# Optimization experiments

Hardware: AMD Instinct MI355X
Metric: run time of the kernel (lower is better)

Reference implementation:

```python
import jax, jax.numpy as jnp
import numpy as np

B, D, CTX, H = 8192, 64, 256, 512  # batch, latent dim (made.nin), context dim, MADE hidden


def _masks(D, H):
    """Standard MADE natural-ordering masks (Germain et al. 2015)."""
    m0 = np.arange(1, D + 1)                 # input degrees 1..D
    mh = (np.arange(H) % (D - 1)) + 1        # hidden degrees 1..D-1
    M1 = (mh[:, None] >= m0[None, :]).astype(np.float32)   # (H, D)
    M2 = (mh[:, None] >= mh[None, :]).astype(np.float32)   # (H, H)
    mo = np.concatenate([m0, m0])            # outputs = [means; pre_scales]
    Mo = (mo[:, None] > mh[None, :]).astype(np.float32)    # (2D, H)
    return jnp.asarray(M1), jnp.asarray(M2), jnp.asarray(Mo)


def setup_inputs() -> dict:
    key = jax.random.key(0)
    ks = jax.random.split(key, 7)
    s = 0.05
    return {
        "context": jax.random.normal(ks[0], (B, CTX), jnp.float32),
        "eps": jax.random.normal(ks[1], (B, D), jnp.float32),  # reparameterization noise
        "W1": jax.random.normal(ks[2], (H, D), jnp.float32) * s,
        "b1": jnp.zeros((H,), jnp.float32),
        "Wc": jax.random.normal(ks[3], (H, CTX), jnp.float32) * s,
        "W2": jax.random.normal(ks[4], (H, H), jnp.float32) * s,
        "b2": jnp.zeros((H,), jnp.float32),
        "Wo": jax.random.normal(ks[5], (2 * D, H), jnp.float32) * s,
        "bo": jnp.zeros((2 * D,), jnp.float32),
    }


def reference(context, eps, W1, b1, Wc, W2, b2, Wo, bo):
    """AutoRegressiveDistribution.rsample (gaussian): D sequential MADE forwards,
    each extracting column i of (mu, softplus(pre_scale)) and sampling z_i."""
    M1, M2, Mo = _masks(D, H)
    W1m, W2m, Wom = (W1 * M1).T, (W2 * M2).T, (Wo * Mo).T
    ctx_h = context @ Wc.T  # context projection is constant across steps

    def step(z, i):
        h = jax.nn.relu(z @ W1m + ctx_h + b1)   # (B, H)
        h = jax.nn.relu(h @ W2m + b2)           # (B, H)
        out = h @ Wom + bo                      # (B, 2D): [means | pre_scales]
        mu_i = out[:, i]
        scale_i = jax.nn.softplus(out[:, D + i])
        z_i = mu_i + scale_i * eps[:, i]        # Normal(mu, scale).rsample()
        z = z.at[:, i].set(z_i)
        return z, (mu_i, scale_i)

    z0 = jnp.zeros((context.shape[0], D), context.dtype)
    z, (mus, scales) = jax.lax.scan(step, z0, jnp.arange(D))
    # state = (z_sample, mu_inferred, scale_inferred), each (B, D)
    return z, mus.T, scales.T
```

## Files before the change

### kernel.cpp

```cpp
#include <hip/hip_runtime.h>
#include <math.h>


typedef float f2 __attribute__((ext_vector_type(2)));

#define Bn 8192
#define Dn 64
#define CTXn 256
#define Hn 512
#define On 128
#define Rn 8

#define WQ_SZ  (64 * 512 * 12)
#define WOQ_SZ (64 * 64 * 20)
#define WCP_SZ (CTXn * Hn)

__device__ __forceinline__ int S_of(int k) {
  if (k <= 0) return 0;
  if (k <= 9) return 9 * (k - 1);
  return 72 + 8 * (k - 9);
}
__device__ __forceinline__ int perm_of(int p, int* degout) {
  int k, t;
  if (p < 72) { k = p / 9 + 1; t = p - (k - 1) * 9; }
  else        { int pp = p - 72; k = pp / 8 + 9; t = pp - (k - 9) * 8; }
  *degout = k;
  return (k - 1) + 63 * t;
}

__global__ void prep_kernel(const float* __restrict__ W1, const float* __restrict__ Wc,
                            const float* __restrict__ W2, const float* __restrict__ Wo,
                            const float* __restrict__ b1, const float* __restrict__ b2,
                            float* __restrict__ Wq, float* __restrict__ Woq,
                            float* __restrict__ WcpT, float* __restrict__ b1p,
                            float* __restrict__ b2p) {
  int idx = blockIdx.x * 256 + threadIdx.x;
  if (idx < WQ_SZ) {
    int i = idx / 6144, rem = idx - i * 6144;
    int q = rem / 12, e = rem - q * 12;
    int sb = (i < 8) ? 9 * i : 8 * i + 8;
    int c  = (i == 63) ? 0 : ((i < 8) ? 9 : 8);
    int dq; int hq = perm_of(q, &dq);
    float v = 0.f;
    if (e < 9) {
      if (e < c && dq >= i + 1) {
        int dp; int hp = perm_of(sb + e, &dp);
        v = W2[hq * Hn + hp];
      }
    } else if (e == 9) {
      if (dq >= i + 1) v = W1[hq * Dn + i];
    }
    Wq[idx] = v;
  } else if (idx < WQ_SZ + WOQ_SZ) {
    int jj = idx - WQ_SZ;
    int i = jj / 1280, rem = jj - i * 1280;
    int j = rem / 20, e = rem - j * 20;
    int sb = (i < 8) ? 9 * i : 8 * i + 8;
    int c  = (i == 63) ? 0 : ((i < 8) ? 9 : 8);
    float v = 0.f;
    int p = -1, o = 0;
    if (e < 9)                { p = e;      o = j; }
    else if (e >= 10 && e < 19) { p = e - 10; o = j + 64; }
    if (p >= 0 && p < c && j >= i + 1) {
      int dp; int hp = perm_of(sb + p, &dp);
      v = Wo[o * Hn + hp];
    }
    Woq[jj] = v;
  } else if (idx < WQ_SZ + WOQ_SZ + WCP_SZ) {
    int jj = idx - (WQ_SZ + WOQ_SZ);
    int cc = jj >> 9, q = jj & 511;
    int dq; int hq = perm_of(q, &dq);
    WcpT[jj] = Wc[hq * CTXn + cc];
  } else if (idx < WQ_SZ + WOQ_SZ + WCP_SZ + 512) {
    int q = idx - (WQ_SZ + WOQ_SZ + WCP_SZ);
    int dq; int hq = perm_of(q, &dq);
    b1p[q] = b1[hq];
  } else if (idx < WQ_SZ + WOQ_SZ + WCP_SZ + 1024) {
    int q = idx - (WQ_SZ + WOQ_SZ + WCP_SZ + 512);
    int dq; int hq = perm_of(q, &dq);
    b2p[q] = b2[hq];
  }
}

__global__ __launch_bounds__(256, 4)
void made_pk_kernel(
    const float* __restrict__ context, const float* __restrict__ WcpT,
    const float* __restrict__ b1p,
    const float* __restrict__ Wq, const float* __restrict__ Woq,
    const float* __restrict__ b2p, const float* __restrict__ bo,
    const float* __restrict__ eps, float* __restrict__ out) {
  __shared__ __align__(16) float ctxR[8][264];
  __shared__ __align__(16) float zcur[8];
  __shared__ __align__(16) float h1g[9][8];
  __shared__ __align__(16) float h2g[9][8];

  int t = threadIdx.x;
  int b0 = blockIdx.x * Rn;
  int rp = t >> 6, l = t & 63;
  int q0 = t, q1 = t + 256;

  int g0 = ((q0 < 72) ? q0 / 9 + 1 : (q0 - 72) / 8 + 9) - 1;
  int g1 = ((q1 - 72) / 8 + 9) - 1;
  int qm = t | 63;
  int gm0s = __builtin_amdgcn_readfirstlane(
      ((qm < 72) ? qm / 9 + 1 : (qm - 72) / 8 + 9) - 1);
  int gm1s = __builtin_amdgcn_readfirstlane(((qm + 256 - 72) / 8 + 9) - 1);

  #pragma unroll
  for (int r = 0; r < 8; ++r)
    ctxR[r][t] = context[(b0 + r) * CTXn + t];
  __syncthreads();

  float acc0[8], acc1[8];
  {
    float bias0 = b1p[q0], bias1 = b1p[q1];
    #pragma unroll
    for (int r = 0; r < 8; ++r) { acc0[r] = bias0; acc1[r] = bias1; }
  }
  {
    const float* wc = WcpT;
    #pragma clang loop unroll(disable)
    for (int c4 = 0; c4 < CTXn / 4; ++c4) {
      float xr[8][4];
      #pragma unroll
      for (int r = 0; r < 8; ++r) {
        float4 x = *(const float4*)&ctxR[r][4 * c4];
        xr[r][0] = x.x; xr[r][1] = x.y; xr[r][2] = x.z; xr[r][3] = x.w;
      }
      #pragma unroll
      for (int k = 0; k < 4; ++k) {
        float w0 = wc[q0], w1 = wc[q1];
        #pragma unroll
        for (int r = 0; r < 8; ++r) {
          acc0[r] = fmaf(xr[r][k], w0, acc0[r]);
          acc1[r] = fmaf(xr[r][k], w1, acc1[r]);
        }
        wc += Hn;
      }
    }
  }

  f2 a10[4], a11[4], a20[4], a21[4];
  #pragma unroll
  for (int r2 = 0; r2 < 4; ++r2) {
    a10[r2] = (f2){acc0[2 * r2], acc0[2 * r2 + 1]};
    a11[r2] = (f2){acc1[2 * r2], acc1[2 * r2 + 1]};
  }
  {
    float bb0 = b2p[q0], bb1 = b2p[q1];
    #pragma unroll
    for (int r2 = 0; r2 < 4; ++r2) {
      a20[r2] = (f2){bb0, bb0};
      a21[r2] = (f2){bb1, bb1};
    }
  }
  f2 ocA = (f2){bo[l], bo[l]};
  f2 ocB = (f2){bo[l + 64], bo[l + 64]};
  f2 ez2 = (f2){eps[(b0 + 2 * rp) * Dn + l], eps[(b0 + 2 * rp + 1) * Dn + l]};
  f2 zs = (f2){0.f, 0.f}, mus = zs, scs = zs;

  const float* wq0p = Wq + (size_t)q0 * 12;
  const float* wq1p = Wq + (size_t)q1 * 12;
  const float* wopp = Woq + (size_t)l * 20;

  #pragma clang loop unroll(disable)
  for (int i = 0; i < Dn; ++i) {
    if (l == i) {
      f2 pre = ocB;
      float sx = fmaxf(pre.x, 0.f) + __logf(1.f + __expf(-fabsf(pre.x)));
      float sy = fmaxf(pre.y, 0.f) + __logf(1.f + __expf(-fabsf(pre.y)));
      f2 sc = (f2){sx, sy};
      f2 z = ocA + sc * ez2;
      *(f2*)&zcur[2 * rp] = z;
      zs = z; mus = ocA; scs = sc;
    }
    __syncthreads();

    int sb = (i < 8) ? 9 * i : 8 * i + 8;
    bool liveB = (i <= gm1s);
    bool liveA = (i <= gm0s);
    float4 A1c0, A1c1, A1c2, A0c0, A0c1, A0c2;
    if (liveB) {
      const float4* a4 = (const float4*)wq1p;
      A1c0 = a4[0]; A1c1 = a4[1]; A1c2 = a4[2];
      if (liveA) {
        const float4* b4 = (const float4*)wq0p;
        A0c0 = b4[0]; A0c1 = b4[1]; A0c2 = b4[2];
      }
      float4 za = *(const float4*)&zcur[0];
      float4 zb = *(const float4*)&zcur[4];
      f2 zc0 = (f2){za.x, za.y}, zc1 = (f2){za.z, za.w};
      f2 zc2 = (f2){zb.x, zb.y}, zc3 = (f2){zb.z, zb.w};
      {
        f2 wv = (f2){A1c2.y, A1c2.y};
        a11[0] += wv * zc0; a11[1] += wv * zc1;
        a11[2] += wv * zc2; a11[3] += wv * zc3;
        if (g1 == i) {
          int pp = q1 - sb;
          float4 h0 = {fmaxf(a11[0].x, 0.f), fmaxf(a11[0].y, 0.f),
                       fmaxf(a11[1].x, 0.f), fmaxf(a11[1].y, 0.f)};
          float4 h1_ = {fmaxf(a11[2].x, 0.f), fmaxf(a11[2].y, 0.f),
                        fmaxf(a11[3].x, 0.f), fmaxf(a11[3].y, 0.f)};
          *(float4*)&h1g[pp][0] = h0; *(float4*)&h1g[pp][4] = h1_;
        }
      }
      if (liveA) {
        f2 wv = (f2){A0c2.y, A0c2.y};
        a10[0] += wv * zc0; a10[1] += wv * zc1;
        a10[2] += wv * zc2; a10[3] += wv * zc3;
        if (g0 == i) {
          int pp = q0 - sb;
          float4 h0 = {fmaxf(a10[0].x, 0.f), fmaxf(a10[0].y, 0.f),
                       fmaxf(a10[1].x, 0.f), fmaxf(a10[1].y, 0.f)};
          float4 h1_ = {fmaxf(a10[2].x, 0.f), fmaxf(a10[2].y, 0.f),
                        fmaxf(a10[3].x, 0.f), fmaxf(a10[3].y, 0.f)};
          *(float4*)&h1g[pp][0] = h0; *(float4*)&h1g[pp][4] = h1_;
        }
      }
    }
    __syncthreads();

    const float4* w4 = (const float4*)wopp;
    float4 B0 = w4[0], B1 = w4[1], B2 = w4[2], B3 = w4[3], B4 = w4[4];

    if (liveB) {
      float wA1[9] = {A1c0.x, A1c0.y, A1c0.z, A1c0.w,
                      A1c1.x, A1c1.y, A1c1.z, A1c1.w, A1c2.x};
      if (liveA) {
        float wA0[9] = {A0c0.x, A0c0.y, A0c0.z, A0c0.w,
                        A0c1.x, A0c1.y, A0c1.z, A0c1.w, A0c2.x};
        #pragma unroll
        for (int p = 0; p < 9; ++p) {
          float4 ha = *(const float4*)&h1g[p][0];
          float4 hb = *(const float4*)&h1g[p][4];
          f2 h0 = (f2){ha.x, ha.y}, h1_ = (f2){ha.z, ha.w};
          f2 h2_ = (f2){hb.x, hb.y}, h3 = (f2){hb.z, hb.w};
          f2 wv1 = (f2){wA1[p], wA1[p]};
          f2 wv0 = (f2){wA0[p], wA0[p]};
          a21[0] += wv1 * h0; a21[1] += wv1 * h1_;
          a21[2] += wv1 * h2_; a21[3] += wv1 * h3;
          a20[0] += wv0 * h0; a20[1] += wv0 * h1_;
          a20[2] += wv0 * h2_; a20[3] += wv0 * h3;
        }
      } else {
        #pragma unroll
        for (int p = 0; p < 9; ++p) {
          float4 ha = *(const float4*)&h1g[p][0];
          float4 hb = *(const float4*)&h1g[p][4];
          f2 h0 = (f2){ha.x, ha.y}, h1_ = (f2){ha.z, ha.w};
          f2 h2_ = (f2){hb.x, hb.y}, h3 = (f2){hb.z, hb.w};
          f2 wv1 = (f2){wA1[p], wA1[p]};
          a21[0] += wv1 * h0; a21[1] += wv1 * h1_;
          a21[2] += wv1 * h2_; a21[3] += wv1 * h3;
        }
      }
      if (g1 == i) {
        int pp = q1 - sb;
        float4 h0 = {fmaxf(a21[0].x, 0.f), fmaxf(a21[0].y, 0.f),
                     fmaxf(a21[1].x, 0.f), fmaxf(a21[1].y, 0.f)};
        float4 h1_ = {fmaxf(a21[2].x, 0.f), fmaxf(a21[2].y, 0.f),
                      fmaxf(a21[3].x, 0.f), fmaxf(a21[3].y, 0.f)};
        *(float4*)&h2g[pp][0] = h0; *(float4*)&h2g[pp][4] = h1_;
      }
      if (liveA && g0 == i) {
        int pp = q0 - sb;
        float4 h0 = {fmaxf(a20[0].x, 0.f), fmaxf(a20[0].y, 0.f),
                     fmaxf(a20[1].x, 0.f), fmaxf(a20[1].y, 0.f)};
        float4 h1_ = {fmaxf(a20[2].x, 0.f), fmaxf(a20[2].y, 0.f),
                      fmaxf(a20[3].x, 0.f), fmaxf(a20[3].y, 0.f)};
        *(float4*)&h2g[pp][0] = h0; *(float4*)&h2g[pp][4] = h1_;
      }
    }
    __syncthreads();

    {
      float wBa[9] = {B0.x, B0.y, B0.z, B0.w, B1.x, B1.y, B1.z, B1.w, B2.x};
      float wBb[9] = {B2.z, B2.w, B3.x, B3.y, B3.z, B3.w, B4.x, B4.y, B4.z};
      #pragma unroll
      for (int p = 0; p < 9; ++p) {
        f2 h = *(const f2*)&h2g[p][2 * rp];
        ocA += (f2){wBa[p], wBa[p]} * h;
        ocB += (f2){wBb[p], wBb[p]} * h;
      }
    }
    wq0p += 6144; wq1p += 6144; wopp += 1280;
  }

  out[(b0 + 2 * rp) * Dn + l] = zs.x;
  out[(b0 + 2 * rp + 1) * Dn + l] = zs.y;
  out[Bn * Dn + (b0 + 2 * rp) * Dn + l] = mus.x;
  out[Bn * Dn + (b0 + 2 * rp + 1) * Dn + l] = mus.y;
  out[2 * Bn * Dn + (b0 + 2 * rp) * Dn + l] = scs.x;
  out[2 * Bn * Dn + (b0 + 2 * rp + 1) * Dn + l] = scs.y;
}

extern "C" void kernel_launch(void* const* d_in, const int* in_sizes, int n_in,
                              void* d_out, int out_size, void* d_ws, size_t ws_size,
                              hipStream_t stream) {
  const float* context = (const float*)d_in[0];
  const float* eps     = (const float*)d_in[1];
  const float* W1      = (const float*)d_in[2];
  const float* b1      = (const float*)d_in[3];
  const float* Wc      = (const float*)d_in[4];
  const float* W2      = (const float*)d_in[5];
  const float* b2      = (const float*)d_in[6];
  const float* Wo      = (const float*)d_in[7];
  const float* bo      = (const float*)d_in[8];
  float* out = (float*)d_out;

  float* ws   = (float*)d_ws;
  float* Wq   = ws;
  float* Woq  = Wq + WQ_SZ;
  float* WcpT = Woq + WOQ_SZ;
  float* b1p  = WcpT + WCP_SZ;
  float* b2p  = b1p + 512;

  int prep_elems = WQ_SZ + WOQ_SZ + WCP_SZ + 1024;
  prep_kernel<<<(prep_elems + 255) / 256, 256, 0, stream>>>(
      W1, Wc, W2, Wo, b1, b2, Wq, Woq, WcpT, b1p, b2p);
  made_pk_kernel<<<Bn / Rn, 256, 0, stream>>>(context, WcpT, b1p, Wq, Woq,
                                              b2p, bo, eps, out);
}
```

Baseline: 239.2 us.

## Use 512-thread blocks with one hidden unit per thread over 16 rows

Reorganizes the per-block work so each of 512 threads owns a single hidden unit and accumulates over 16 batch rows, where before 256 threads each owned two units over 8 rows. Grid size halves and weight loads per row are amortized over twice as many rows. Each step's early-exit liveness check is now per wave on a single unit. The output stage still indexes 64 lanes by 2*rp rows, and with rp ranging 0..7 this covers the 16 rows. The cost is more accumulator registers per thread and larger barrier groups.

```diff
diff --git a/kernel.cpp b/kernel.cpp
--- a/kernel.cpp
+++ b/kernel.cpp
@@ -9,17 +9,12 @@
 #define CTXn 256
 #define Hn 512
 #define On 128
-#define Rn 8
+#define Rn 16
 
 #define WQ_SZ  (64 * 512 * 12)
 #define WOQ_SZ (64 * 64 * 20)
 #define WCP_SZ (CTXn * Hn)
 
-__device__ __forceinline__ int S_of(int k) {
-  if (k <= 0) return 0;
-  if (k <= 9) return 9 * (k - 1);
-  return 72 + 8 * (k - 9);
-}
 __device__ __forceinline__ int perm_of(int p, int* degout) {
   int k, t;
   if (p < 72) { k = p / 9 + 1; t = p - (k - 1) * 9; }
@@ -59,7 +54,7 @@
     int c  = (i == 63) ? 0 : ((i < 8) ? 9 : 8);
     float v = 0.f;
     int p = -1, o = 0;
-    if (e < 9)                { p = e;      o = j; }
+    if (e < 9)                  { p = e;      o = j; }
     else if (e >= 10 && e < 19) { p = e - 10; o = j + 64; }
     if (p >= 0 && p < c && j >= i + 1) {
       int dp; int hp = perm_of(sb + p, &dp);
@@ -82,85 +77,76 @@
   }
 }
 
-__global__ __launch_bounds__(256, 4)
+__global__ __launch_bounds__(512, 2)
 void made_pk_kernel(
     const float* __restrict__ context, const float* __restrict__ WcpT,
     const float* __restrict__ b1p,
     const float* __restrict__ Wq, const float* __restrict__ Woq,
     const float* __restrict__ b2p, const float* __restrict__ bo,
     const float* __restrict__ eps, float* __restrict__ out) {
-  __shared__ __align__(16) float ctxR[8][264];
-  __shared__ __align__(16) float zcur[8];
-  __shared__ __align__(16) float h1g[9][8];
-  __shared__ __align__(16) float h2g[9][8];
+  __shared__ __align__(16) float ctxR[Rn][264];
+  __shared__ __align__(16) float zcur[Rn];
+  __shared__ __align__(16) float h1g[9][Rn];
+  __shared__ __align__(16) float h2g[9][Rn];
 
   int t = threadIdx.x;
   int b0 = blockIdx.x * Rn;
-  int rp = t >> 6, l = t & 63;
-  int q0 = t, q1 = t + 256;
-
-  int g0 = ((q0 < 72) ? q0 / 9 + 1 : (q0 - 72) / 8 + 9) - 1;
-  int g1 = ((q1 - 72) / 8 + 9) - 1;
+  int q = t;
+  int l = t & 63, rp = t >> 6;
+
+  int fstep = (q < 72) ? q / 9 : (q - 72) / 8 + 8;
   int qm = t | 63;
-  int gm0s = __builtin_amdgcn_readfirstlane(
-      ((qm < 72) ? qm / 9 + 1 : (qm - 72) / 8 + 9) - 1);
-  int gm1s = __builtin_amdgcn_readfirstlane(((qm + 256 - 72) / 8 + 9) - 1);
-
-  #pragma unroll
-  for (int r = 0; r < 8; ++r)
-    ctxR[r][t] = context[(b0 + r) * CTXn + t];
+  int gmax = __builtin_amdgcn_readfirstlane(
+      (qm < 72) ? qm / 9 : (qm - 72) / 8 + 8);
+
+  for (int idx = t; idx < Rn * CTXn; idx += 512) {
+    int r = idx >> 8, cc = idx & 255;
+    ctxR[r][cc] = context[(b0 + r) * CTXn + cc];
+  }
   __syncthreads();
 
-  float acc0[8], acc1[8];
+  float acc[Rn];
   {
-    float bias0 = b1p[q0], bias1 = b1p[q1];
+    float bias = b1p[q];
     #pragma unroll
-    for (int r = 0; r < 8; ++r) { acc0[r] = bias0; acc1[r] = bias1; }
-  }
-  {
+    for (int r = 0; r < Rn; ++r) acc[r] = bias;
+  }
+  #pragma clang loop unroll(disable)
+  for (int half = 0; half < 2; ++half) {
     const float* wc = WcpT;
     #pragma clang loop unroll(disable)
     for (int c4 = 0; c4 < CTXn / 4; ++c4) {
       float xr[8][4];
       #pragma unroll
       for (int r = 0; r < 8; ++r) {
-        float4 x = *(const float4*)&ctxR[r][4 * c4];
+        float4 x = *(const float4*)&ctxR[8 * half + r][4 * c4];
         xr[r][0] = x.x; xr[r][1] = x.y; xr[r][2] = x.z; xr[r][3] = x.w;
       }
       #pragma unroll
       for (int k = 0; k < 4; ++k) {
-        float w0 = wc[q0], w1 = wc[q1];
-        #pragma unroll
-        for (int r = 0; r < 8; ++r) {
-          acc0[r] = fmaf(xr[r][k], w0, acc0[r]);
-          acc1[r] = fmaf(xr[r][k], w1, acc1[r]);
-        }
+        float w0 = wc[q];
+        #pragma unroll
+        for (int r = 0; r < 8; ++r)
+          acc[8 * half + r] = fmaf(xr[r][k], w0, acc[8 * half + r]);
         wc += Hn;
       }
     }
   }
 
-  f2 a10[4], a11[4], a20[4], a21[4];
+  f2 a1[8], a2[8];
   #pragma unroll
-  for (int r2 = 0; r2 < 4; ++r2) {
-    a10[r2] = (f2){acc0[2 * r2], acc0[2 * r2 + 1]};
-    a11[r2] = (f2){acc1[2 * r2], acc1[2 * r2 + 1]};
-  }
+  for (int r2 = 0; r2 < 8; ++r2) a1[r2] = (f2){acc[2 * r2], acc[2 * r2 + 1]};
   {
-    float bb0 = b2p[q0], bb1 = b2p[q1];
+    float bb = b2p[q];
     #pragma unroll
-    for (int r2 = 0; r2 < 4; ++r2) {
-      a20[r2] = (f2){bb0, bb0};
-      a21[r2] = (f2){bb1, bb1};
-    }
+    for (int r2 = 0; r2 < 8; ++r2) a2[r2] = (f2){bb, bb};
   }
   f2 ocA = (f2){bo[l], bo[l]};
   f2 ocB = (f2){bo[l + 64], bo[l + 64]};
   f2 ez2 = (f2){eps[(b0 + 2 * rp) * Dn + l], eps[(b0 + 2 * rp + 1) * Dn + l]};
   f2 zs = (f2){0.f, 0.f}, mus = zs, scs = zs;
 
-  const float* wq0p = Wq + (size_t)q0 * 12;
-  const float* wq1p = Wq + (size_t)q1 * 12;
+  const float* wqp = Wq + (size_t)q * 12;
   const float* wopp = Woq + (size_t)l * 20;
 
   #pragma clang loop unroll(disable)
@@ -177,44 +163,28 @@
     __syncthreads();
 
     int sb = (i < 8) ? 9 * i : 8 * i + 8;
-    bool liveB = (i <= gm1s);
-    bool liveA = (i <= gm0s);
-    float4 A1c0, A1c1, A1c2, A0c0, A0c1, A0c2;
-    if (liveB) {
-      const float4* a4 = (const float4*)wq1p;
-      A1c0 = a4[0]; A1c1 = a4[1]; A1c2 = a4[2];
-      if (liveA) {
-        const float4* b4 = (const float4*)wq0p;
-        A0c0 = b4[0]; A0c1 = b4[1]; A0c2 = b4[2];
-      }
+    bool live = (i <= gmax);
+    float4 A0, A1, A2;
+    if (live) {
+      const float4* a4 = (const float4*)wqp;
+      A0 = a4[0]; A1 = a4[1]; A2 = a4[2];
       float4 za = *(const float4*)&zcur[0];
       float4 zb = *(const float4*)&zcur[4];
-      f2 zc0 = (f2){za.x, za.y}, zc1 = (f2){za.z, za.w};
-      f2 zc2 = (f2){zb.x, zb.y}, zc3 = (f2){zb.z, zb.w};
-      {
-        f2 wv = (f2){A1c2.y, A1c2.y};
-        a11[0] += wv * zc0; a11[1] += wv * zc1;
-        a11[2] += wv * zc2; a11[3] += wv * zc3;
-        if (g1 == i) {
-          int pp = q1 - sb;
-          float4 h0 = {fmaxf(a11[0].x, 0.f), fmaxf(a11[0].y, 0.f),
-                       fmaxf(a11[1].x, 0.f), fmaxf(a11[1].y, 0.f)};
-          float4 h1_ = {fmaxf(a11[2].x, 0.f), fmaxf(a11[2].y, 0.f),
-                        fmaxf(a11[3].x, 0.f), fmaxf(a11[3].y, 0.f)};
-          *(float4*)&h1g[pp][0] = h0; *(float4*)&h1g[pp][4] = h1_;
-        }
-      }
-      if (liveA) {
-        f2 wv = (f2){A0c2.y, A0c2.y};
-        a10[0] += wv * zc0; a10[1] += wv * zc1;
-        a10[2] += wv * zc2; a10[3] += wv * zc3;
-        if (g0 == i) {
-          int pp = q0 - sb;
-          float4 h0 = {fmaxf(a10[0].x, 0.f), fmaxf(a10[0].y, 0.f),
-                       fmaxf(a10[1].x, 0.f), fmaxf(a10[1].y, 0.f)};
-          float4 h1_ = {fmaxf(a10[2].x, 0.f), fmaxf(a10[2].y, 0.f),
-                        fmaxf(a10[3].x, 0.f), fmaxf(a10[3].y, 0.f)};
-          *(float4*)&h1g[pp][0] = h0; *(float4*)&h1g[pp][4] = h1_;
+      float4 zc_ = *(const float4*)&zcur[8];
+      float4 zd = *(const float4*)&zcur[12];
+      f2 zc[8] = {(f2){za.x, za.y}, (f2){za.z, za.w},
+                  (f2){zb.x, zb.y}, (f2){zb.z, zb.w},
+                  (f2){zc_.x, zc_.y}, (f2){zc_.z, zc_.w},
+                  (f2){zd.x, zd.y}, (f2){zd.z, zd.w}};
+      f2 wv = (f2){A2.y, A2.y};
+      #pragma unroll
+      for (int r2 = 0; r2 < 8; ++r2) a1[r2] += wv * zc[r2];
+      if (fstep == i) {
+        int pp = q - sb;
+        #pragma unroll
+        for (int r2 = 0; r2 < 8; ++r2) {
+          f2 h = (f2){fmaxf(a1[r2].x, 0.f), fmaxf(a1[r2].y, 0.f)};
+          *(f2*)&h1g[pp][2 * r2] = h;
         }
       }
     }
@@ -223,52 +193,29 @@
     const float4* w4 = (const float4*)wopp;
     float4 B0 = w4[0], B1 = w4[1], B2 = w4[2], B3 = w4[3], B4 = w4[4];
 
-    if (liveB) {
-      float wA1[9] = {A1c0.x, A1c0.y, A1c0.z, A1c0.w,
-                      A1c1.x, A1c1.y, A1c1.z, A1c1.w, A1c2.x};
-      if (liveA) {
-        float wA0[9] = {A0c0.x, A0c0.y, A0c0.z, A0c0.w,
-                        A0c1.x, A0c1.y, A0c1.z, A0c1.w, A0c2.x};
-        #pragma unroll
-        for (int p = 0; p < 9; ++p) {
-          float4 ha = *(const float4*)&h1g[p][0];
-          float4 hb = *(const float4*)&h1g[p][4];
-          f2 h0 = (f2){ha.x, ha.y}, h1_ = (f2){ha.z, ha.w};
-          f2 h2_ = (f2){hb.x, hb.y}, h3 = (f2){hb.z, hb.w};
-          f2 wv1 = (f2){wA1[p], wA1[p]};
-          f2 wv0 = (f2){wA0[p], wA0[p]};
-          a21[0] += wv1 * h0; a21[1] += wv1 * h1_;
-          a21[2] += wv1 * h2_; a21[3] += wv1 * h3;
-          a20[0] += wv0 * h0; a20[1] += wv0 * h1_;
-          a20[2] += wv0 * h2_; a20[3] += wv0 * h3;
+    if (live) {
+      float wA[9] = {A0.x, A0.y, A0.z, A0.w, A1.x, A1.y, A1.z, A1.w, A2.x};
+      #pragma unroll
+      for (int p = 0; p < 9; ++p) {
+        float4 ha = *(const float4*)&h1g[p][0];
+        float4 hb = *(const float4*)&h1g[p][4];
+        float4 hc = *(const float4*)&h1g[p][8];
+        float4 hd = *(const float4*)&h1g[p][12];
+        f2 h[8] = {(f2){ha.x, ha.y}, (f2){ha.z, ha.w},
+                   (f2){hb.x, hb.y}, (f2){hb.z, hb.w},
+                   (f2){hc.x, hc.y}, (f2){hc.z, hc.w},
+                   (f2){hd.x, hd.y}, (f2){hd.z, hd.w}};
+        f2 wv = (f2){wA[p], wA[p]};
+        #pragma unroll
+        for (int r2 = 0; r2 < 8; ++r2) a2[r2] += wv * h[r2];
+      }
+      if (fstep == i) {
+        int pp = q - sb;
+        #pragma unroll
+        for (int r2 = 0; r2 < 8; ++r2) {
+          f2 h = (f2){fmaxf(a2[r2].x, 0.f), fmaxf(a2[r2].y, 0.f)};
+          *(f2*)&h2g[pp][2 * r2] = h;
         }
-      } else {
-        #pragma unroll
-        for (int p = 0; p < 9; ++p) {
-          float4 ha = *(const float4*)&h1g[p][0];
-          float4 hb = *(const float4*)&h1g[p][4];
-          f2 h0 = (f2){ha.x, ha.y}, h1_ = (f2){ha.z, ha.w};
-          f2 h2_ = (f2){hb.x, hb.y}, h3 = (f2){hb.z, hb.w};
-          f2 wv1 = (f2){wA1[p], wA1[p]};
-          a21[0] += wv1 * h0; a21[1] += wv1 * h1_;
-          a21[2] += wv1 * h2_; a21[3] += wv1 * h3;
-        }
-      }
-      if (g1 == i) {
-        int pp = q1 - sb;
-        float4 h0 = {fmaxf(a21[0].x, 0.f), fmaxf(a21[0].y, 0.f),
-                     fmaxf(a21[1].x, 0.f), fmaxf(a21[1].y, 0.f)};
-        float4 h1_ = {fmaxf(a21[2].x, 0.f), fmaxf(a21[2].y, 0.f),
-                      fmaxf(a21[3].x, 0.f), fmaxf(a21[3].y, 0.f)};
-        *(float4*)&h2g[pp][0] = h0; *(float4*)&h2g[pp][4] = h1_;
-      }
-      if (liveA && g0 == i) {
-        int pp = q0 - sb;
-        float4 h0 = {fmaxf(a20[0].x, 0.f), fmaxf(a20[0].y, 0.f),
-                     fmaxf(a20[1].x, 0.f), fmaxf(a20[1].y, 0.f)};
-        float4 h1_ = {fmaxf(a20[2].x, 0.f), fmaxf(a20[2].y, 0.f),
-                      fmaxf(a20[3].x, 0.f), fmaxf(a20[3].y, 0.f)};
-        *(float4*)&h2g[pp][0] = h0; *(float4*)&h2g[pp][4] = h1_;
       }
     }
     __syncthreads();
@@ -283,7 +230,7 @@
         ocB += (f2){wBb[p], wBb[p]} * h;
       }
     }
-    wq0p += 6144; wq1p += 6144; wopp += 1280;
+    wqp += 6144; wopp += 1280;
   }
 
   out[(b0 + 2 * rp) * Dn + l] = zs.x;
@@ -318,6 +265,6 @@
   int prep_elems = WQ_SZ + WOQ_SZ + WCP_SZ + 1024;
   prep_kernel<<<(prep_elems + 255) / 256, 256, 0, stream>>>(
       W1, Wc, W2, Wo, b1, b2, Wq, Woq, WcpT, b1p, b2p);
-  made_pk_kernel<<<Bn / Rn, 256, 0, stream>>>(context, WcpT, b1p, Wq, Woq,
+  made_pk_kernel<<<Bn / Rn, 512, 0, stream>>>(context, WcpT, b1p, Wq, Woq,
                                               b2p, bo, eps, out);
 }
```

Result: slower. 265.3 us (+10.9%).
